# Performance work log

Measured on AMD Instinct MI355X. Metric: run time of the kernel, lower is better.

The kernel has to match this reference:

```python
import jax, jax.numpy as jnp
import numpy as np

N = 100000
E = 1600000
D = 64    # input feat
H = 128   # hidden_channels
O = 64    # out_channels


def _sage(x, src, dst, Wl, bl, Wr, n_nodes):
    # mean-aggregate neighbor features: out[i] = mean_{(j->i)} x[j]
    msg = x[src]                                   # [E, F] gather
    agg = jax.ops.segment_sum(msg, dst, num_segments=n_nodes)
    cnt = jax.ops.segment_sum(jnp.ones((src.shape[0], 1), x.dtype), dst,
                              num_segments=n_nodes)
    mean = agg / jnp.maximum(cnt, 1.0)
    # SAGEConv: lin_l(aggr) + lin_r(x)  (bias lives in lin_l)
    return mean @ Wl + bl + x @ Wr


def setup_inputs() -> dict:
    key = jax.random.key(0)
    ks = jax.random.split(key, 12)
    s = lambda fan_in: 1.0 / np.sqrt(fan_in)
    x = jax.random.normal(ks[0], (N, D), dtype=jnp.float32)
    edge_index = jax.random.randint(ks[1], (2, E), 0, N, dtype=jnp.int64)
    return {
        "x": x,
        "edge_index": edge_index,
        "W1l": jax.random.uniform(ks[2], (D, H), jnp.float32, -s(D), s(D)),
        "b1": jax.random.uniform(ks[3], (H,), jnp.float32, -s(D), s(D)),
        "W1r": jax.random.uniform(ks[4], (D, H), jnp.float32, -s(D), s(D)),
        "Wlin1": jax.random.uniform(ks[5], (H, H), jnp.float32, -s(H), s(H)),
        "blin1": jax.random.uniform(ks[6], (H,), jnp.float32, -s(H), s(H)),
        "W2l": jax.random.uniform(ks[7], (H, H), jnp.float32, -s(H), s(H)),
        "b2": jax.random.uniform(ks[8], (H,), jnp.float32, -s(H), s(H)),
        "W2r": jax.random.uniform(ks[9], (H, H), jnp.float32, -s(H), s(H)),
        "Wlin2": jax.random.uniform(ks[10], (H, O), jnp.float32, -s(H), s(H)),
        "blin2": jax.random.uniform(ks[11], (O,), jnp.float32, -s(H), s(H)),
    }


def reference(x, edge_index, W1l, b1, W1r, Wlin1, blin1, W2l, b2, W2r, Wlin2, blin2):
    src, dst = edge_index[0], edge_index[1]
    h = jax.nn.relu(_sage(x, src, dst, W1l, b1, W1r, N))
    h = jax.nn.relu(h @ Wlin1 + blin1)
    h = jax.nn.relu(_sage(h, src, dst, W2l, b2, W2r, N))
    return h @ Wlin2 + blin2
```

## Files before the change

kernel.cpp:

```cpp
#include <hip/hip_runtime.h>
#include <cstddef>

static constexpr int NN = 100000;
static constexpr int NE = 1600000;
static constexpr int NODE_SHIFT = 8;
static constexpr int NB = (NN + 255) >> NODE_SHIFT;
static constexpr int CHUNK = 8192;
static constexpr int NCH = (NE + CHUNK - 1) / CHUNK;

typedef _Float16 f16x8 __attribute__((ext_vector_type(8)));
typedef float f32x4  __attribute__((ext_vector_type(4)));

__device__ __forceinline__ void acc8h(const uint4& v, float* a) {
    union { uint4 u; _Float16 h[8]; } t; t.u = v;
#pragma unroll
    for (int j = 0; j < 8; j++) a[j] += (float)t.h[j];
}


__global__ void bucket_count(const int* __restrict__ eidx, int* __restrict__ bcnt) {
    __shared__ int h[NB];
    for (int i = threadIdx.x; i < NB; i += 256) h[i] = 0;
    __syncthreads();
    int base = blockIdx.x * CHUNK;
    int end = min(base + CHUNK, NE);
    for (int e = base + threadIdx.x; e < end; e += 256)
        atomicAdd(&h[eidx[NE + e] >> NODE_SHIFT], 1);
    __syncthreads();
    for (int i = threadIdx.x; i < NB; i += 256)
        if (h[i]) atomicAdd(&bcnt[i], h[i]);
}

__global__ void bucket_scan(const int* __restrict__ bcnt, int* __restrict__ bbase,
                            int* __restrict__ bcur, int* __restrict__ row_ptr) {
    __shared__ int s[512];
    int t = threadIdx.x;
    int v = (t < NB) ? bcnt[t] : 0;
    s[t] = v; __syncthreads();
    for (int off = 1; off < 512; off <<= 1) {
        int x = (t >= off) ? s[t - off] : 0;
        __syncthreads();
        s[t] += x;
        __syncthreads();
    }
    if (t < NB) { int e = s[t] - v; bbase[t] = e; bcur[t] = e; }
    if (t == 0) { bbase[NB] = NE; row_ptr[NN] = NE; }
}

__global__ void bucket_scatter(const int* __restrict__ eidx, int* __restrict__ bcur,
                               uint2* __restrict__ pairs) {
    __shared__ int h[NB];
    __shared__ int cur[NB];
    __shared__ int off[NB];
    for (int i = threadIdx.x; i < NB; i += 256) { h[i] = 0; cur[i] = 0; }
    __syncthreads();
    int base = blockIdx.x * CHUNK;
    int end = min(base + CHUNK, NE);
    for (int e = base + threadIdx.x; e < end; e += 256)
        atomicAdd(&h[eidx[NE + e] >> NODE_SHIFT], 1);
    __syncthreads();
    for (int i = threadIdx.x; i < NB; i += 256)
        off[i] = h[i] ? atomicAdd(&bcur[i], h[i]) : 0;
    __syncthreads();
    for (int e = base + threadIdx.x; e < end; e += 256) {
        int d = eidx[NE + e], s = eidx[e];
        int b = d >> NODE_SHIFT;
        int p = atomicAdd(&cur[b], 1);
        pairs[off[b] + p] = make_uint2((unsigned)s, (unsigned)d);
    }
}

__launch_bounds__(256)
__global__ void bucket_csr(const uint2* __restrict__ pairs, const int* __restrict__ bbase,
                           int* __restrict__ row_ptr, int* __restrict__ ecsr) {
    __shared__ int hist[256];
    __shared__ int scn[256];
    __shared__ int cur[256];
    int b = blockIdx.x, t = threadIdx.x;
    int ebeg = bbase[b], eend = bbase[b + 1];
    int node0 = b << NODE_SHIFT;
    hist[t] = 0;
    __syncthreads();
    for (int e = ebeg + t; e < eend; e += 256)
        atomicAdd(&hist[pairs[e].y & 255u], 1);
    __syncthreads();
    int v = hist[t];
    scn[t] = v; __syncthreads();
    for (int off = 1; off < 256; off <<= 1) {
        int x = (t >= off) ? scn[t - off] : 0;
        __syncthreads();
        scn[t] += x;
        __syncthreads();
    }
    int excl = scn[t] - v;
    int node = node0 + t;
    if (node < NN) row_ptr[node] = ebeg + excl;
    cur[t] = excl;
    __syncthreads();
    for (int e = ebeg + t; e < eend; e += 256) {
        uint2 pr = pairs[e];
        int p = atomicAdd(&cur[pr.y & 255u], 1);
        ecsr[ebeg + p] = (int)pr.x;
    }
}

__global__ void conv_fused(const float* __restrict__ x,
                           const float* __restrict__ W1l, const float* __restrict__ W1r,
                           const float* __restrict__ Wlin1, const float* __restrict__ W2l,
                           const float* __restrict__ W2r, const float* __restrict__ Wlin2,
                           unsigned short* __restrict__ bufP, unsigned short* __restrict__ Wt1,
                           unsigned short* __restrict__ Wtl1, unsigned short* __restrict__ Wt2,
                           unsigned short* __restrict__ Wtf, int* __restrict__ bcnt) {
    int bid = blockIdx.x, t = threadIdx.x;
    union { _Float16 h; unsigned short u; } cv;
    if (bid < 25000) {
        int idx = bid * 256 + t;
        int r = idx >> 6, c = idx & 63;
        cv.h = (_Float16)x[idx];
        bufP[(size_t)r * 128 + 64 + c] = cv.u;
    } else if (bid >= 25288) {
        int i = (bid - 25288) * 256 + t;
        if (i < NB) bcnt[i] = 0;
    } else {
        int b = bid - 25000;
        const float* W; unsigned short* Wt; int K, C, wld, kbase, base;
        if (b < 32)       { W = W1l;   Wt = Wt1;  K = 64;  C = 128; wld = 128; kbase = 0;   base = b; }
        else if (b < 64)  { W = W1r;   Wt = Wt1;  K = 64;  C = 128; wld = 128; kbase = 64;  base = b - 32; }
        else if (b < 128) { W = Wlin1; Wt = Wtl1; K = 128; C = 128; wld = 128; kbase = 0;   base = b - 64; }
        else if (b < 192) { W = W2l;   Wt = Wt2;  K = 128; C = 128; wld = 256; kbase = 0;   base = b - 128; }
        else if (b < 256) { W = W2r;   Wt = Wt2;  K = 128; C = 128; wld = 256; kbase = 128; base = b - 192; }
        else              { W = Wlin2; Wt = Wtf;  K = 128; C = 64;  wld = 128; kbase = 0;   base = b - 256; }
        int idx = base * 256 + t;
        if (idx < K * C) {
            int k = idx / C, c = idx % C;
            cv.h = (_Float16)W[idx];
            Wt[(size_t)c * wld + kbase + k] = cv.u;
        }
    }
}


__launch_bounds__(256)
__global__ void agg1(const unsigned short* __restrict__ xp, const int* __restrict__ row_ptr,
                     const int* __restrict__ ecsr, unsigned short* __restrict__ outp) {
    constexpr int TPN = 8;
    int node = blockIdx.x * (256 / TPN) + threadIdx.x / TPN;
    int lane = threadIdx.x % TPN;
    if (node >= NN) return;
    int beg = row_ptr[node], end = row_ptr[node + 1];

    float a0[8] = {0,0,0,0,0,0,0,0}, a1[8] = {0,0,0,0,0,0,0,0};
    float a2[8] = {0,0,0,0,0,0,0,0}, a3[8] = {0,0,0,0,0,0,0,0};
    int i = beg;
    for (; i + 4 <= end; i += 4) {
        int s0 = ecsr[i], s1 = ecsr[i + 1], s2 = ecsr[i + 2], s3 = ecsr[i + 3];
        uint4 v0 = *(const uint4*)&xp[(size_t)s0 * 128 + 64 + lane * 8];
        uint4 v1 = *(const uint4*)&xp[(size_t)s1 * 128 + 64 + lane * 8];
        uint4 v2 = *(const uint4*)&xp[(size_t)s2 * 128 + 64 + lane * 8];
        uint4 v3 = *(const uint4*)&xp[(size_t)s3 * 128 + 64 + lane * 8];
        acc8h(v0, a0); acc8h(v1, a1); acc8h(v2, a2); acc8h(v3, a3);
    }
    for (; i < end; i++) {
        uint4 v0 = *(const uint4*)&xp[(size_t)ecsr[i] * 128 + 64 + lane * 8];
        acc8h(v0, a0);
    }
    int deg = end - beg;
    float r = (deg > 0) ? 1.f / (float)deg : 0.f;
    union { uint4 u; _Float16 h[8]; } o;
#pragma unroll
    for (int j = 0; j < 8; j++)
        o.h[j] = (_Float16)((a0[j] + a1[j] + a2[j] + a3[j]) * r);
    *(uint4*)(outp + (size_t)node * 128 + lane * 8) = o.u;
}

__launch_bounds__(256)
__global__ void agg2(const unsigned short* __restrict__ hbuf, const int* __restrict__ row_ptr,
                     const int* __restrict__ ecsr, unsigned short* __restrict__ outp) {
    constexpr int TPN = 16;
    int node = blockIdx.x * (256 / TPN) + threadIdx.x / TPN;
    int lane = threadIdx.x % TPN;
    if (node >= NN) return;
    int beg = row_ptr[node], end = row_ptr[node + 1];

    float a0[8] = {0,0,0,0,0,0,0,0}, a1[8] = {0,0,0,0,0,0,0,0};
    float a2[8] = {0,0,0,0,0,0,0,0}, a3[8] = {0,0,0,0,0,0,0,0};
    int i = beg;
    for (; i + 4 <= end; i += 4) {
        int s0 = ecsr[i], s1 = ecsr[i + 1], s2 = ecsr[i + 2], s3 = ecsr[i + 3];
        uint4 v0 = *(const uint4*)&hbuf[(size_t)s0 * 256 + 128 + lane * 8];
        uint4 v1 = *(const uint4*)&hbuf[(size_t)s1 * 256 + 128 + lane * 8];
        uint4 v2 = *(const uint4*)&hbuf[(size_t)s2 * 256 + 128 + lane * 8];
        uint4 v3 = *(const uint4*)&hbuf[(size_t)s3 * 256 + 128 + lane * 8];
        acc8h(v0, a0); acc8h(v1, a1); acc8h(v2, a2); acc8h(v3, a3);
    }
    for (; i < end; i++) {
        uint4 v0 = *(const uint4*)&hbuf[(size_t)ecsr[i] * 256 + 128 + lane * 8];
        acc8h(v0, a0);
    }
    int deg = end - beg;
    float r = (deg > 0) ? 1.f / (float)deg : 0.f;
    union { uint4 u; _Float16 h[8]; } o;
#pragma unroll
    for (int j = 0; j < 8; j++)
        o.h[j] = (_Float16)((a0[j] + a1[j] + a2[j] + a3[j]) * r);
    *(uint4*)(outp + (size_t)node * 256 + lane * 8) = o.u;
}

template<int K, int C, bool RELU, bool F16OUT>
__launch_bounds__(256, 4)
__global__ void gemm_f16(const unsigned short* __restrict__ A, int lda,
                         const unsigned short* __restrict__ Wt,
                         const float* __restrict__ bias,
                         unsigned short* __restrict__ outp, int old_, int obase,
                         float* __restrict__ outf) {
    constexpr int BM  = 128;
    constexpr int NKC = K / 64;
    constexpr int RT  = (C == 128) ? 4 : 2;
    __shared__ unsigned short As[BM * 72];
    __shared__ unsigned short Ws[C * 72];

    const int tid  = threadIdx.x;
    const int lane = tid & 63, wave = tid >> 6;
    const int lrow = lane & 15, quad = lane >> 4;
    const int wrow0 = (C == 128) ? (wave >> 1) * 64 : wave * 32;
    const int wcol0 = (C == 128) ? (wave & 1) * 64 : 0;
    const int row0  = blockIdx.x * BM;

    f32x4 acc[RT][4];
#pragma unroll
    for (int a = 0; a < RT; a++)
#pragma unroll
        for (int b = 0; b < 4; b++) acc[a][b] = (f32x4){0.f, 0.f, 0.f, 0.f};

#pragma unroll 1
    for (int it = 0; it < NKC; ++it) {
        int base = it * 64;
        for (int t = tid; t < BM * 8; t += 256) {
            int r = t >> 3, c8 = (t & 7) * 8;
            int gr = row0 + r;
            uint4 v = make_uint4(0u, 0u, 0u, 0u);
            if (gr < NN) v = *(const uint4*)&A[(size_t)gr * lda + base + c8];
            *(uint4*)&As[r * 72 + c8] = v;
        }
        for (int t = tid; t < C * 8; t += 256) {
            int wr = t >> 3, c8 = (t & 7) * 8;
            *(uint4*)&Ws[wr * 72 + c8] = *(const uint4*)&Wt[(size_t)wr * K + base + c8];
        }
        __syncthreads();
#pragma unroll
        for (int ks = 0; ks < 2; ++ks) {
            f16x8 af[RT], bfr[4];
#pragma unroll
            for (int rt = 0; rt < RT; rt++)
                af[rt] = *(const f16x8*)&As[(wrow0 + rt * 16 + lrow) * 72 + ks * 32 + quad * 8];
#pragma unroll
            for (int ct = 0; ct < 4; ct++)
                bfr[ct] = *(const f16x8*)&Ws[(wcol0 + ct * 16 + lrow) * 72 + ks * 32 + quad * 8];
#pragma unroll
            for (int rt = 0; rt < RT; rt++)
#pragma unroll
                for (int ct = 0; ct < 4; ct++)
                    acc[rt][ct] = __builtin_amdgcn_mfma_f32_16x16x32_f16(
                        af[rt], bfr[ct], acc[rt][ct], 0, 0, 0);
        }
        __syncthreads();
    }

    float bcol[4];
#pragma unroll
    for (int ct = 0; ct < 4; ct++) bcol[ct] = bias[wcol0 + ct * 16 + lrow];
#pragma unroll
    for (int rt = 0; rt < RT; rt++) {
#pragma unroll
        for (int ct = 0; ct < 4; ct++) {
#pragma unroll
            for (int r = 0; r < 4; r++) {
                int grow = row0 + wrow0 + rt * 16 + quad * 4 + r;
                if (grow < NN) {
                    int col = wcol0 + ct * 16 + lrow;
                    float v = acc[rt][ct][r] + bcol[ct];
                    if (RELU) v = fmaxf(v, 0.f);
                    if (F16OUT) {
                        union { _Float16 h; unsigned short u; } cv;
                        cv.h = (_Float16)v;
                        outp[(size_t)grow * old_ + obase + col] = cv.u;
                    } else {
                        outf[(size_t)grow * C + col] = v;
                    }
                }
            }
        }
    }
}


extern "C" void kernel_launch(void* const* d_in, const int* in_sizes, int n_in,
                              void* d_out, int out_size, void* d_ws, size_t ws_size,
                              hipStream_t stream) {
    const float* x     = (const float*)d_in[0];
    const int*   eidx  = (const int*)d_in[1];
    const float* W1l   = (const float*)d_in[2];
    const float* b1    = (const float*)d_in[3];
    const float* W1r   = (const float*)d_in[4];
    const float* Wlin1 = (const float*)d_in[5];
    const float* blin1 = (const float*)d_in[6];
    const float* W2l   = (const float*)d_in[7];
    const float* b2    = (const float*)d_in[8];
    const float* W2r   = (const float*)d_in[9];
    const float* Wlin2 = (const float*)d_in[10];
    const float* blin2 = (const float*)d_in[11];
    float* out = (float*)d_out;
    (void)in_sizes; (void)n_in; (void)out_size; (void)ws_size;

    char* ws = (char*)d_ws;
    size_t off = 0;
    auto alloc = [&](size_t bytes) -> void* {
        void* p = ws + off;
        off = (off + bytes + 255) & ~(size_t)255;
        return p;
    };
    int* bcnt    = (int*)alloc((size_t)NB * 4);
    int* bbase   = (int*)alloc((size_t)(NB + 1) * 4);
    int* bcur    = (int*)alloc((size_t)NB * 4);
    int* row_ptr = (int*)alloc((size_t)(NN + 1) * 4);
    int* ecsr    = (int*)alloc((size_t)NE * 4);
    uint2* pairs = (uint2*)alloc((size_t)NE * 8);
    unsigned short* Wt1  = (unsigned short*)alloc((size_t)128 * 128 * 2);
    unsigned short* Wtl1 = (unsigned short*)alloc((size_t)128 * 128 * 2);
    unsigned short* Wt2  = (unsigned short*)alloc((size_t)128 * 256 * 2);
    unsigned short* Wtf  = (unsigned short*)alloc((size_t)64  * 128 * 2);
    unsigned short* bufP = (unsigned short*)alloc((size_t)NN * 128 * 2);
    unsigned short* bufQ = (unsigned short*)alloc((size_t)NN * 256 * 2);
    unsigned short* bufR = (unsigned short*)alloc((size_t)NN * 128 * 2);

    conv_fused<<<25290, 256, 0, stream>>>(x, W1l, W1r, Wlin1, W2l, W2r, Wlin2,
                                          bufP, Wt1, Wtl1, Wt2, Wtf, bcnt);

    bucket_count<<<NCH, 256, 0, stream>>>(eidx, bcnt);
    bucket_scan<<<1, 512, 0, stream>>>(bcnt, bbase, bcur, row_ptr);
    bucket_scatter<<<NCH, 256, 0, stream>>>(eidx, bcur, pairs);
    bucket_csr<<<NB, 256, 0, stream>>>(pairs, bbase, row_ptr, ecsr);

    agg1<<<(NN + 31) / 32, 256, 0, stream>>>(bufP, row_ptr, ecsr, bufP);

    const int GB128 = (NN + 127) / 128;

    gemm_f16<128, 128, true, true><<<GB128, 256, 0, stream>>>(
        bufP, 128, Wt1, b1, bufR, 128, 0, nullptr);
    gemm_f16<128, 128, true, true><<<GB128, 256, 0, stream>>>(
        bufR, 128, Wtl1, blin1, bufQ, 256, 128, nullptr);
    agg2<<<(NN + 15) / 16, 256, 0, stream>>>(bufQ, row_ptr, ecsr, bufQ);
    gemm_f16<256, 128, true, true><<<GB128, 256, 0, stream>>>(
        bufQ, 256, Wt2, b2, bufR, 128, 0, nullptr);
    gemm_f16<128, 64, false, false><<<GB128, 256, 0, stream>>>(
        bufR, 128, Wtf, blin2, nullptr, 0, 0, out);
}
```

Baseline: 312.2 us.

## Fuse back-to-back GEMM pairs so the intermediate stays in shared memory

Two consecutive GEMM launches, layer-1 SAGE linear followed by lin1 and layer-2 SAGE linear followed by the final linear, are merged into one kernel per pair. The first GEMM's ReLU'd fp16 output tile is written to LDS and consumed directly by the second GEMM, so the intermediate buffer bufR never goes through global memory. This removes two launches and an NN×128 fp16 write and read round-trip. In exchange LDS use per block goes up, since there are two extra 128×72 tiles, and launch bounds drop to 2 blocks per CU, which lowers occupancy.

```diff
diff --git a/kernel.cpp b/kernel.cpp
--- a/kernel.cpp
+++ b/kernel.cpp
@@ -206,34 +206,38 @@
     *(uint4*)(outp + (size_t)node * 256 + lane * 8) = o.u;
 }
 
-template<int K, int C, bool RELU, bool F16OUT>
-__launch_bounds__(256, 4)
-__global__ void gemm_f16(const unsigned short* __restrict__ A, int lda,
-                         const unsigned short* __restrict__ Wt,
-                         const float* __restrict__ bias,
-                         unsigned short* __restrict__ outp, int old_, int obase,
-                         float* __restrict__ outf) {
-    constexpr int BM  = 128;
-    constexpr int NKC = K / 64;
-    constexpr int RT  = (C == 128) ? 4 : 2;
+template<int K1, int C2, bool RELU2, bool F16OUT2>
+__launch_bounds__(256, 2)
+__global__ void gemm2x(const unsigned short* __restrict__ A, int lda,
+                       const unsigned short* __restrict__ Wta,
+                       const float* __restrict__ ba,
+                       const unsigned short* __restrict__ Wtb,
+                       const float* __restrict__ bb,
+                       unsigned short* __restrict__ outp, int old_, int obase,
+                       float* __restrict__ outf) {
+    constexpr int BM   = 128;
+    constexpr int NKC1 = K1 / 64;
     __shared__ unsigned short As[BM * 72];
-    __shared__ unsigned short Ws[C * 72];
+    __shared__ unsigned short Ws[128 * 72];
+    __shared__ unsigned short Hs0[BM * 72];
+    __shared__ unsigned short Hs1[BM * 72];
 
     const int tid  = threadIdx.x;
     const int lane = tid & 63, wave = tid >> 6;
     const int lrow = lane & 15, quad = lane >> 4;
-    const int wrow0 = (C == 128) ? (wave >> 1) * 64 : wave * 32;
-    const int wcol0 = (C == 128) ? (wave & 1) * 64 : 0;
-    const int row0  = blockIdx.x * BM;
-
-    f32x4 acc[RT][4];
-#pragma unroll
-    for (int a = 0; a < RT; a++)
+    const int row0 = blockIdx.x * BM;
+
+    const int wrow0 = (wave >> 1) * 64;
+    const int wcol0 = (wave & 1) * 64;
+
+    f32x4 acc[4][4];
+#pragma unroll
+    for (int a = 0; a < 4; a++)
 #pragma unroll
         for (int b = 0; b < 4; b++) acc[a][b] = (f32x4){0.f, 0.f, 0.f, 0.f};
 
 #pragma unroll 1
-    for (int it = 0; it < NKC; ++it) {
+    for (int it = 0; it < NKC1; ++it) {
         int base = it * 64;
         for (int t = tid; t < BM * 8; t += 256) {
             int r = t >> 3, c8 = (t & 7) * 8;
@@ -242,22 +246,22 @@
             if (gr < NN) v = *(const uint4*)&A[(size_t)gr * lda + base + c8];
             *(uint4*)&As[r * 72 + c8] = v;
         }
-        for (int t = tid; t < C * 8; t += 256) {
+        for (int t = tid; t < 128 * 8; t += 256) {
             int wr = t >> 3, c8 = (t & 7) * 8;
-            *(uint4*)&Ws[wr * 72 + c8] = *(const uint4*)&Wt[(size_t)wr * K + base + c8];
+            *(uint4*)&Ws[wr * 72 + c8] = *(const uint4*)&Wta[(size_t)wr * K1 + base + c8];
         }
         __syncthreads();
 #pragma unroll
         for (int ks = 0; ks < 2; ++ks) {
-            f16x8 af[RT], bfr[4];
-#pragma unroll
-            for (int rt = 0; rt < RT; rt++)
+            f16x8 af[4], bfr[4];
+#pragma unroll
+            for (int rt = 0; rt < 4; rt++)
                 af[rt] = *(const f16x8*)&As[(wrow0 + rt * 16 + lrow) * 72 + ks * 32 + quad * 8];
 #pragma unroll
             for (int ct = 0; ct < 4; ct++)
                 bfr[ct] = *(const f16x8*)&Ws[(wcol0 + ct * 16 + lrow) * 72 + ks * 32 + quad * 8];
 #pragma unroll
-            for (int rt = 0; rt < RT; rt++)
+            for (int rt = 0; rt < 4; rt++)
 #pragma unroll
                 for (int ct = 0; ct < 4; ct++)
                     acc[rt][ct] = __builtin_amdgcn_mfma_f32_16x16x32_f16(
@@ -266,26 +270,84 @@
         __syncthreads();
     }
 
-    float bcol[4];
-#pragma unroll
-    for (int ct = 0; ct < 4; ct++) bcol[ct] = bias[wcol0 + ct * 16 + lrow];
-#pragma unroll
-    for (int rt = 0; rt < RT; rt++) {
+    {
+        unsigned short* Hp = (wcol0 == 0) ? Hs0 : Hs1;
+        float bc[4];
+#pragma unroll
+        for (int ct = 0; ct < 4; ct++) bc[ct] = ba[wcol0 + ct * 16 + lrow];
+#pragma unroll
+        for (int rt = 0; rt < 4; rt++) {
+#pragma unroll
+            for (int ct = 0; ct < 4; ct++) {
+#pragma unroll
+                for (int r = 0; r < 4; r++) {
+                    int rl = wrow0 + rt * 16 + quad * 4 + r;
+                    float v = fmaxf(acc[rt][ct][r] + bc[ct], 0.f);
+                    union { _Float16 h; unsigned short u; } cv;
+                    cv.h = (_Float16)v;
+                    Hp[rl * 72 + ct * 16 + lrow] = cv.u;
+                }
+            }
+        }
+    }
+
+    constexpr int RT2 = (C2 == 128) ? 4 : 2;
+    const int wrow2 = (C2 == 128) ? (wave >> 1) * 64 : wave * 32;
+    const int wcol2 = (C2 == 128) ? (wave & 1) * 64 : 0;
+
+    f32x4 acc2[RT2][4];
+#pragma unroll
+    for (int a = 0; a < RT2; a++)
+#pragma unroll
+        for (int b = 0; b < 4; b++) acc2[a][b] = (f32x4){0.f, 0.f, 0.f, 0.f};
+
+#pragma unroll
+    for (int it = 0; it < 2; ++it) {
+        const unsigned short* Hp = it ? Hs1 : Hs0;
+        for (int t = tid; t < C2 * 8; t += 256) {
+            int wr = t >> 3, c8 = (t & 7) * 8;
+            *(uint4*)&Ws[wr * 72 + c8] = *(const uint4*)&Wtb[(size_t)wr * 128 + it * 64 + c8];
+        }
+        __syncthreads();
+#pragma unroll
+        for (int ks = 0; ks < 2; ++ks) {
+            f16x8 af[RT2], bfr[4];
+#pragma unroll
+            for (int rt = 0; rt < RT2; rt++)
+                af[rt] = *(const f16x8*)&Hp[(wrow2 + rt * 16 + lrow) * 72 + ks * 32 + quad * 8];
+#pragma unroll
+            for (int ct = 0; ct < 4; ct++)
+                bfr[ct] = *(const f16x8*)&Ws[(wcol2 + ct * 16 + lrow) * 72 + ks * 32 + quad * 8];
+#pragma unroll
+            for (int rt = 0; rt < RT2; rt++)
+#pragma unroll
+                for (int ct = 0; ct < 4; ct++)
+                    acc2[rt][ct] = __builtin_amdgcn_mfma_f32_16x16x32_f16(
+                        af[rt], bfr[ct], acc2[rt][ct], 0, 0, 0);
+        }
+        __syncthreads();
+    }
+
+    float bc2[4];
+#pragma unroll
+    for (int ct = 0; ct < 4; ct++) bc2[ct] = bb[wcol2 + ct * 16 + lrow];
+#pragma unroll
+    for (int rt = 0; rt < RT2; rt++) {
 #pragma unroll
         for (int ct = 0; ct < 4; ct++) {
 #pragma unroll
             for (int r = 0; r < 4; r++) {
-                int grow = row0 + wrow0 + rt * 16 + quad * 4 + r;
+                int grow = row0 + wrow2 + rt * 16 + quad * 4 + r;
                 if (grow < NN) {
-                    int col = wcol0 + ct * 16 + lrow;
-                    float v = acc[rt][ct][r] + bcol[ct];
-                    if (RELU) v = fmaxf(v, 0.f);
-                    if (F16OUT) {
+                    int col = wcol2 + ct * 16 + lrow;
+                    float v = acc2[rt][ct][r] + bc2[ct];
+                    if (RELU2) v = fmaxf(v, 0.f);
+                    if (F16OUT2) {
                         union { _Float16 h; unsigned short u; } cv;
                         cv.h = (_Float16)v;
                         outp[(size_t)grow * old_ + obase + col] = cv.u;
                     } else {
-                        outf[(size_t)grow * C + col] = v;
+                        outf[(size_t)grow * C2 + col] = v;
                     }
                 }
             }
@@ -331,7 +393,6 @@
     unsigned short* Wtf  = (unsigned short*)alloc((size_t)64  * 128 * 2);
     unsigned short* bufP = (unsigned short*)alloc((size_t)NN * 128 * 2);
     unsigned short* bufQ = (unsigned short*)alloc((size_t)NN * 256 * 2);
-    unsigned short* bufR = (unsigned short*)alloc((size_t)NN * 128 * 2);
 
     conv_fused<<<25290, 256, 0, stream>>>(x, W1l, W1r, Wlin1, W2l, W2r, Wlin2,
                                           bufP, Wt1, Wtl1, Wt2, Wtf, bcnt);
@@ -345,13 +406,11 @@
 
     const int GB128 = (NN + 127) / 128;
 
-    gemm_f16<128, 128, true, true><<<GB128, 256, 0, stream>>>(
-        bufP, 128, Wt1, b1, bufR, 128, 0, nullptr);
-    gemm_f16<128, 128, true, true><<<GB128, 256, 0, stream>>>(
-        bufR, 128, Wtl1, blin1, bufQ, 256, 128, nullptr);
+    gemm2x<128, 128, true, true><<<GB128, 256, 0, stream>>>(
+        bufP, 128, Wt1, b1, Wtl1, blin1, bufQ, 256, 128, nullptr);
+
     agg2<<<(NN + 15) / 16, 256, 0, stream>>>(bufQ, row_ptr, ecsr, bufQ);
-    gemm_f16<256, 128, true, true><<<GB128, 256, 0, stream>>>(
-        bufQ, 256, Wt2, b2, bufR, 128, 0, nullptr);
-    gemm_f16<128, 64, false, false><<<GB128, 256, 0, stream>>>(
-        bufR, 128, Wtf, blin2, nullptr, 0, 0, out);
-}
+
+    gemm2x<256, 64, false, false><<<GB128, 256, 0, stream>>>(
+        bufQ, 256, Wt2, b2, Wtf, blin2, nullptr, 0, 0, out);
+}
```

Result: no change. 314.0 us, median of 2 (+0.6%).

## Fuse neighbor mean aggregation into the SAGE GEMM kernels

Applied to the files above, without the earlier changes.

Removes the separate agg1 and agg2 kernels and performs the mean aggregation inside the GEMM blocks that consume it. In layer 1 the aggregated rows go straight into shared memory, which avoids a global write and re-read. In layer 2 the aggregate is still written to global memory, but within the same launch. This saves launches and some memory traffic. In exchange, the gather runs with far fewer threads in flight per node batch and a serial loop over row groups, so latency hiding for the random gathers may suffer.

```diff
diff --git a/kernel.cpp b/kernel.cpp
--- a/kernel.cpp
+++ b/kernel.cpp
@@ -139,73 +139,6 @@
     }
 }
 
-
-__launch_bounds__(256)
-__global__ void agg1(const unsigned short* __restrict__ xp, const int* __restrict__ row_ptr,
-                     const int* __restrict__ ecsr, unsigned short* __restrict__ outp) {
-    constexpr int TPN = 8;
-    int node = blockIdx.x * (256 / TPN) + threadIdx.x / TPN;
-    int lane = threadIdx.x % TPN;
-    if (node >= NN) return;
-    int beg = row_ptr[node], end = row_ptr[node + 1];
-
-    float a0[8] = {0,0,0,0,0,0,0,0}, a1[8] = {0,0,0,0,0,0,0,0};
-    float a2[8] = {0,0,0,0,0,0,0,0}, a3[8] = {0,0,0,0,0,0,0,0};
-    int i = beg;
-    for (; i + 4 <= end; i += 4) {
-        int s0 = ecsr[i], s1 = ecsr[i + 1], s2 = ecsr[i + 2], s3 = ecsr[i + 3];
-        uint4 v0 = *(const uint4*)&xp[(size_t)s0 * 128 + 64 + lane * 8];
-        uint4 v1 = *(const uint4*)&xp[(size_t)s1 * 128 + 64 + lane * 8];
-        uint4 v2 = *(const uint4*)&xp[(size_t)s2 * 128 + 64 + lane * 8];
-        uint4 v3 = *(const uint4*)&xp[(size_t)s3 * 128 + 64 + lane * 8];
-        acc8h(v0, a0); acc8h(v1, a1); acc8h(v2, a2); acc8h(v3, a3);
-    }
-    for (; i < end; i++) {
-        uint4 v0 = *(const uint4*)&xp[(size_t)ecsr[i] * 128 + 64 + lane * 8];
-        acc8h(v0, a0);
-    }
-    int deg = end - beg;
-    float r = (deg > 0) ? 1.f / (float)deg : 0.f;
-    union { uint4 u; _Float16 h[8]; } o;
-#pragma unroll
-    for (int j = 0; j < 8; j++)
-        o.h[j] = (_Float16)((a0[j] + a1[j] + a2[j] + a3[j]) * r);
-    *(uint4*)(outp + (size_t)node * 128 + lane * 8) = o.u;
-}
-
-__launch_bounds__(256)
-__global__ void agg2(const unsigned short* __restrict__ hbuf, const int* __restrict__ row_ptr,
-                     const int* __restrict__ ecsr, unsigned short* __restrict__ outp) {
-    constexpr int TPN = 16;
-    int node = blockIdx.x * (256 / TPN) + threadIdx.x / TPN;
-    int lane = threadIdx.x % TPN;
-    if (node >= NN) return;
-    int beg = row_ptr[node], end = row_ptr[node + 1];
-
-    float a0[8] = {0,0,0,0,0,0,0,0}, a1[8] = {0,0,0,0,0,0,0,0};
-    float a2[8] = {0,0,0,0,0,0,0,0}, a3[8] = {0,0,0,0,0,0,0,0};
-    int i = beg;
-    for (; i + 4 <= end; i += 4) {
-        int s0 = ecsr[i], s1 = ecsr[i + 1], s2 = ecsr[i + 2], s3 = ecsr[i + 3];
-        uint4 v0 = *(const uint4*)&hbuf[(size_t)s0 * 256 + 128 + lane * 8];
-        uint4 v1 = *(const uint4*)&hbuf[(size_t)s1 * 256 + 128 + lane * 8];
-        uint4 v2 = *(const uint4*)&hbuf[(size_t)s2 * 256 + 128 + lane * 8];
-        uint4 v3 = *(const uint4*)&hbuf[(size_t)s3 * 256 + 128 + lane * 8];
-        acc8h(v0, a0); acc8h(v1, a1); acc8h(v2, a2); acc8h(v3, a3);
-    }
-    for (; i < end; i++) {
-        uint4 v0 = *(const uint4*)&hbuf[(size_t)ecsr[i] * 256 + 128 + lane * 8];
-        acc8h(v0, a0);
-    }
-    int deg = end - beg;
-    float r = (deg > 0) ? 1.f / (float)deg : 0.f;
-    union { uint4 u; _Float16 h[8]; } o;
-#pragma unroll
-    for (int j = 0; j < 8; j++)
-        o.h[j] = (_Float16)((a0[j] + a1[j] + a2[j] + a3[j]) * r);
-    *(uint4*)(outp + (size_t)node * 256 + lane * 8) = o.u;
-}
-
 template<int K, int C, bool RELU, bool F16OUT>
 __launch_bounds__(256, 4)
 __global__ void gemm_f16(const unsigned short* __restrict__ A, int lda,
@@ -287,6 +220,239 @@
                     } else {
                         outf[(size_t)grow * C + col] = v;
                     }
+                }
+            }
+        }
+    }
+}
+
+__launch_bounds__(256, 4)
+__global__ void gemm_s1(const unsigned short* __restrict__ xp,
+                        const int* __restrict__ row_ptr, const int* __restrict__ ecsr,
+                        const unsigned short* __restrict__ Wt,
+                        const float* __restrict__ bias,
+                        unsigned short* __restrict__ outp) {
+    constexpr int BM = 128;
+    __shared__ unsigned short As[BM * 72];
+    __shared__ unsigned short Ws[128 * 72];
+
+    const int tid  = threadIdx.x;
+    const int lane = tid & 63, wave = tid >> 6;
+    const int lrow = lane & 15, quad = lane >> 4;
+    const int wrow0 = (wave >> 1) * 64;
+    const int wcol0 = (wave & 1) * 64;
+    const int row0  = blockIdx.x * BM;
+
+    {
+        const int l = tid & 7;
+        const int rb = tid >> 3;
+#pragma unroll 1
+        for (int p = 0; p < 4; p++) {
+            int r = p * 32 + rb;
+            int node = row0 + r;
+            union { uint4 u; _Float16 h[8]; } o;
+            if (node < NN) {
+                int beg = row_ptr[node], end = row_ptr[node + 1];
+                float a0[8] = {0,0,0,0,0,0,0,0}, a1[8] = {0,0,0,0,0,0,0,0};
+                float a2[8] = {0,0,0,0,0,0,0,0}, a3[8] = {0,0,0,0,0,0,0,0};
+                int i = beg;
+                for (; i + 4 <= end; i += 4) {
+                    int s0 = ecsr[i], s1 = ecsr[i + 1], s2 = ecsr[i + 2], s3 = ecsr[i + 3];
+                    uint4 v0 = *(const uint4*)&xp[(size_t)s0 * 128 + 64 + l * 8];
+                    uint4 v1 = *(const uint4*)&xp[(size_t)s1 * 128 + 64 + l * 8];
+                    uint4 v2 = *(const uint4*)&xp[(size_t)s2 * 128 + 64 + l * 8];
+                    uint4 v3 = *(const uint4*)&xp[(size_t)s3 * 128 + 64 + l * 8];
+                    acc8h(v0, a0); acc8h(v1, a1); acc8h(v2, a2); acc8h(v3, a3);
+                }
+                for (; i < end; i++) {
+                    uint4 v0 = *(const uint4*)&xp[(size_t)ecsr[i] * 128 + 64 + l * 8];
+                    acc8h(v0, a0);
+                }
+                int deg = end - beg;
+                float rr = (deg > 0) ? 1.f / (float)deg : 0.f;
+#pragma unroll
+                for (int j = 0; j < 8; j++)
+                    o.h[j] = (_Float16)((a0[j] + a1[j] + a2[j] + a3[j]) * rr);
+            } else {
+                o.u = make_uint4(0u, 0u, 0u, 0u);
+            }
+            *(uint4*)&As[r * 72 + l * 8] = o.u;
+        }
+    }
+
+    f32x4 acc[4][4];
+#pragma unroll
+    for (int a = 0; a < 4; a++)
+#pragma unroll
+        for (int b = 0; b < 4; b++) acc[a][b] = (f32x4){0.f, 0.f, 0.f, 0.f};
+
+#pragma unroll 1
+    for (int it = 0; it < 2; ++it) {
+        int base = it * 64;
+        if (it == 1) {
+            for (int t = tid; t < BM * 8; t += 256) {
+                int r = t >> 3, c8 = (t & 7) * 8;
+                int gr = row0 + r;
+                uint4 v = make_uint4(0u, 0u, 0u, 0u);
+                if (gr < NN) v = *(const uint4*)&xp[(size_t)gr * 128 + 64 + c8];
+                *(uint4*)&As[r * 72 + c8] = v;
+            }
+        }
+        for (int t = tid; t < 128 * 8; t += 256) {
+            int wr = t >> 3, c8 = (t & 7) * 8;
+            *(uint4*)&Ws[wr * 72 + c8] = *(const uint4*)&Wt[(size_t)wr * 128 + base + c8];
+        }
+        __syncthreads();
+#pragma unroll
+        for (int ks = 0; ks < 2; ++ks) {
+            f16x8 af[4], bfr[4];
+#pragma unroll
+            for (int rt = 0; rt < 4; rt++)
+                af[rt] = *(const f16x8*)&As[(wrow0 + rt * 16 + lrow) * 72 + ks * 32 + quad * 8];
+#pragma unroll
+            for (int ct = 0; ct < 4; ct++)
+                bfr[ct] = *(const f16x8*)&Ws[(wcol0 + ct * 16 + lrow) * 72 + ks * 32 + quad * 8];
+#pragma unroll
+            for (int rt = 0; rt < 4; rt++)
+#pragma unroll
+                for (int ct = 0; ct < 4; ct++)
+                    acc[rt][ct] = __builtin_amdgcn_mfma_f32_16x16x32_f16(
+                        af[rt], bfr[ct], acc[rt][ct], 0, 0, 0);
+        }
+        __syncthreads();
+    }
+
+    float bcol[4];
+#pragma unroll
+    for (int ct = 0; ct < 4; ct++) bcol[ct] = bias[wcol0 + ct * 16 + lrow];
+#pragma unroll
+    for (int rt = 0; rt < 4; rt++) {
+#pragma unroll
+        for (int ct = 0; ct < 4; ct++) {
+#pragma unroll
+            for (int r = 0; r < 4; r++) {
+                int grow = row0 + wrow0 + rt * 16 + quad * 4 + r;
+                if (grow < NN) {
+                    int col = wcol0 + ct * 16 + lrow;
+                    float v = fmaxf(acc[rt][ct][r] + bcol[ct], 0.f);
+                    union { _Float16 h; unsigned short u; } cv;
+                    cv.h = (_Float16)v;
+                    outp[(size_t)grow * 128 + col] = cv.u;
+                }
+            }
+        }
+    }
+}
+
+__launch_bounds__(256, 4)
+__global__ void gemm_s2(unsigned short* __restrict__ hq,
+                        const int* __restrict__ row_ptr, const int* __restrict__ ecsr,
+                        const unsigned short* __restrict__ Wt,
+                        const float* __restrict__ bias,
+                        unsigned short* __restrict__ outp) {
+    constexpr int BM = 128;
+    __shared__ unsigned short As[BM * 72];
+    __shared__ unsigned short Ws[128 * 72];
+
+    const int tid  = threadIdx.x;
+    const int lane = tid & 63, wave = tid >> 6;
+    const int lrow = lane & 15, quad = lane >> 4;
+    const int wrow0 = (wave >> 1) * 64;
+    const int wcol0 = (wave & 1) * 64;
+    const int row0  = blockIdx.x * BM;
+
+    {
+        const int l = tid & 15;
+        const int rb = tid >> 4;
+#pragma unroll 1
+        for (int p = 0; p < 8; p++) {
+            int r = p * 16 + rb;
+            int node = row0 + r;
+            if (node < NN) {
+                int beg = row_ptr[node], end = row_ptr[node + 1];
+                float a0[8] = {0,0,0,0,0,0,0,0}, a1[8] = {0,0,0,0,0,0,0,0};
+                float a2[8] = {0,0,0,0,0,0,0,0}, a3[8] = {0,0,0,0,0,0,0,0};
+                int i = beg;
+                for (; i + 4 <= end; i += 4) {
+                    int s0 = ecsr[i], s1 = ecsr[i + 1], s2 = ecsr[i + 2], s3 = ecsr[i + 3];
+                    uint4 v0 = *(const uint4*)&hq[(size_t)s0 * 256 + 128 + l * 8];
+                    uint4 v1 = *(const uint4*)&hq[(size_t)s1 * 256 + 128 + l * 8];
+                    uint4 v2 = *(const uint4*)&hq[(size_t)s2 * 256 + 128 + l * 8];
+                    uint4 v3 = *(const uint4*)&hq[(size_t)s3 * 256 + 128 + l * 8];
+                    acc8h(v0, a0); acc8h(v1, a1); acc8h(v2, a2); acc8h(v3, a3);
+                }
+                for (; i < end; i++) {
+                    uint4 v0 = *(const uint4*)&hq[(size_t)ecsr[i] * 256 + 128 + l * 8];
+                    acc8h(v0, a0);
+                }
+                int deg = end - beg;
+                float rr = (deg > 0) ? 1.f / (float)deg : 0.f;
+                union { uint4 u; _Float16 h[8]; } o;
+#pragma unroll
+                for (int j = 0; j < 8; j++)
+                    o.h[j] = (_Float16)((a0[j] + a1[j] + a2[j] + a3[j]) * rr);
+                *(uint4*)(hq + (size_t)node * 256 + l * 8) = o.u;
+            }
+        }
+    }
+    __syncthreads();
+
+    f32x4 acc[4][4];
+#pragma unroll
+    for (int a = 0; a < 4; a++)
+#pragma unroll
+        for (int b = 0; b < 4; b++) acc[a][b] = (f32x4){0.f, 0.f, 0.f, 0.f};
+
+#pragma unroll 1
+    for (int it = 0; it < 4; ++it) {
+        int base = it * 64;
+        for (int t = tid; t < BM * 8; t += 256) {
+            int r = t >> 3, c8 = (t & 7) * 8;
+            int gr = row0 + r;
+            uint4 v = make_uint4(0u, 0u, 0u, 0u);
+            if (gr < NN) v = *(const uint4*)&hq[(size_t)gr * 256 + base + c8];
+            *(uint4*)&As[r * 72 + c8] = v;
+        }
+        for (int t = tid; t < 128 * 8; t += 256) {
+            int wr = t >> 3, c8 = (t & 7) * 8;
+            *(uint4*)&Ws[wr * 72 + c8] = *(const uint4*)&Wt[(size_t)wr * 256 + base + c8];
+        }
+        __syncthreads();
+#pragma unroll
+        for (int ks = 0; ks < 2; ++ks) {
+            f16x8 af[4], bfr[4];
+#pragma unroll
+            for (int rt = 0; rt < 4; rt++)
+                af[rt] = *(const f16x8*)&As[(wrow0 + rt * 16 + lrow) * 72 + ks * 32 + quad * 8];
+#pragma unroll
+            for (int ct = 0; ct < 4; ct++)
+                bfr[ct] = *(const f16x8*)&Ws[(wcol0 + ct * 16 + lrow) * 72 + ks * 32 + quad * 8];
+#pragma unroll
+            for (int rt = 0; rt < 4; rt++)
+#pragma unroll
+                for (int ct = 0; ct < 4; ct++)
+                    acc[rt][ct] = __builtin_amdgcn_mfma_f32_16x16x32_f16(
+                        af[rt], bfr[ct], acc[rt][ct], 0, 0, 0);
+        }
+        __syncthreads();
+    }
+
+    float bcol[4];
+#pragma unroll
+    for (int ct = 0; ct < 4; ct++) bcol[ct] = bias[wcol0 + ct * 16 + lrow];
+#pragma unroll
+    for (int rt = 0; rt < 4; rt++) {
+#pragma unroll
+        for (int ct = 0; ct < 4; ct++) {
+#pragma unroll
+            for (int r = 0; r < 4; r++) {
+                int grow = row0 + wrow0 + rt * 16 + quad * 4 + r;
+                if (grow < NN) {
+                    int col = wcol0 + ct * 16 + lrow;
+                    float v = fmaxf(acc[rt][ct][r] + bcol[ct], 0.f);
+                    union { _Float16 h; unsigned short u; } cv;
+                    cv.h = (_Float16)v;
+                    outp[(size_t)grow * 128 + col] = cv.u;
                 }
             }
         }
@@ -341,17 +507,12 @@
     bucket_scatter<<<NCH, 256, 0, stream>>>(eidx, bcur, pairs);
     bucket_csr<<<NB, 256, 0, stream>>>(pairs, bbase, row_ptr, ecsr);
 
-    agg1<<<(NN + 31) / 32, 256, 0, stream>>>(bufP, row_ptr, ecsr, bufP);
-
     const int GB128 = (NN + 127) / 128;
 
-    gemm_f16<128, 128, true, true><<<GB128, 256, 0, stream>>>(
-        bufP, 128, Wt1, b1, bufR, 128, 0, nullptr);
+    gemm_s1<<<GB128, 256, 0, stream>>>(bufP, row_ptr, ecsr, Wt1, b1, bufR);
     gemm_f16<128, 128, true, true><<<GB128, 256, 0, stream>>>(
         bufR, 128, Wtl1, blin1, bufQ, 256, 128, nullptr);
-    agg2<<<(NN + 15) / 16, 256, 0, stream>>>(bufQ, row_ptr, ecsr, bufQ);
-    gemm_f16<256, 128, true, true><<<GB128, 256, 0, stream>>>(
-        bufQ, 256, Wt2, b2, bufR, 128, 0, nullptr);
+    gemm_s2<<<GB128, 256, 0, stream>>>(bufQ, row_ptr, ecsr, Wt2, b2, bufR);
     gemm_f16<128, 64, false, false><<<GB128, 256, 0, stream>>>(
         bufR, 128, Wtf, blin2, nullptr, 0, 0, out);
 }
```

New measurement: 317.4 us. About the same (+1.7%).
